# Performance work log

Measured on AMD Instinct MI355X. Metric: run time of the kernel, lower is better.

The kernel has to match this reference:

```python
import jax, jax.numpy as jnp
import numpy as np

N_HEAD = 16
D_K = 64
D_V = 64
EMBED = 1024
BATCH = 4
SEQ = 2048

def setup_inputs() -> dict:
    key = jax.random.key(0)
    ks = jax.random.split(key, 12)
    s = lambda d: 1.0 / np.sqrt(d)
    u = lambda k, shape, d: jax.random.uniform(k, shape, jnp.float32, -s(d), s(d))
    return {
        'z': jax.random.normal(ks[0], (BATCH, SEQ, EMBED), jnp.float32),
        'wq': u(ks[1], (EMBED, D_K), D_K),
        'wk': u(ks[2], (EMBED, D_K), D_K),
        'wv': u(ks[3], (EMBED, D_V), D_V),
        'fcq_w': u(ks[4], (D_K, N_HEAD * D_K), D_K),
        'fcq_b': u(ks[5], (N_HEAD * D_K,), N_HEAD * D_K),
        'fck_w': u(ks[6], (D_K, N_HEAD * D_K), D_K),
        'fck_b': u(ks[7], (N_HEAD * D_K,), N_HEAD * D_K),
        'fcv_w': u(ks[8], (D_V, N_HEAD * D_V), D_V),
        'fcv_b': u(ks[9], (N_HEAD * D_V,), N_HEAD * D_V),
        'fco_w': u(ks[10], (N_HEAD * D_V, EMBED), EMBED),
        'fco_b': u(ks[11], (EMBED,), EMBED),
    }

def reference(z, wq, wk, wv, fcq_w, fcq_b, fck_w, fck_b, fcv_w, fcv_b, fco_w, fco_b):
    b, n, _ = z.shape
    scale = jnp.sqrt(jnp.float32(D_K))
    # bottleneck projections then per-head expansion
    q = (z @ wq) @ fcq_w + fcq_b  # [b, n, H*dk]
    k = (z @ wk) @ fck_w + fck_b  # [b, n, H*dk]
    v = (z @ wv) @ fcv_w + fcv_b  # [b, n, H*dv]
    q = q.reshape(b, n, N_HEAD, D_K)
    k = k.reshape(b, n, N_HEAD, D_K)
    v = v.reshape(b, n, N_HEAD, D_V)
    scores = jnp.einsum('bihd,bjhd->bhij', q, k) / scale  # [b, H, n, n]
    attn = jax.nn.softmax(scores, axis=-1)
    out = jnp.einsum('bhij,bjhd->bihd', attn, v)  # [b, n, H, dv]
    out = out.reshape(b, n, N_HEAD * D_V)
    return out @ fco_w + fco_b  # [b, n, embed]
```

## Files before the change

kernel.cpp:

```cpp
#include <hip/hip_runtime.h>


typedef __bf16 bf16x8 __attribute__((ext_vector_type(8)));
typedef __bf16 bf16x4 __attribute__((ext_vector_type(4)));
typedef __bf16 bf16x2 __attribute__((ext_vector_type(2)));
typedef float floatx4 __attribute__((ext_vector_type(4)));
typedef float floatx16 __attribute__((ext_vector_type(16)));
typedef unsigned int uintx4 __attribute__((ext_vector_type(4)));
typedef unsigned int uintx2 __attribute__((ext_vector_type(2)));

#define SW64(row, col) (((row) << 6) | (((((col) >> 3) ^ ((row) & 7) ^ (((row) >> 3) & 7)) << 3) | ((col) & 7)))

#if __has_builtin(__builtin_amdgcn_exp2f)
__device__ __forceinline__ float fast_exp2(float x) { return __builtin_amdgcn_exp2f(x); }
#else
__device__ __forceinline__ float fast_exp2(float x) { return exp2f(x); }
#endif

__device__ __forceinline__ unsigned int pack_bf16(float lo, float hi) {
    bf16x2 w; w[0] = (__bf16)lo; w[1] = (__bf16)hi;
    return __builtin_bit_cast(unsigned int, w);
}
__device__ __forceinline__ unsigned int pack2(__bf16 lo, __bf16 hi) {
    bf16x2 w; w[0] = lo; w[1] = hi;
    return __builtin_bit_cast(unsigned int, w);
}
#if __has_builtin(__builtin_amdgcn_permlane32_swap)
__device__ __forceinline__ void xchg(unsigned int& X, unsigned int& Y, int) {
    uintx2 r = __builtin_amdgcn_permlane32_swap(X, Y, false, false);
    X = r[0]; Y = r[1];
}
#else
__device__ __forceinline__ void xchg(unsigned int& X, unsigned int& Y, int hl) {
    unsigned int sX = (unsigned int)__shfl_xor((int)X, 32);
    unsigned int sY = (unsigned int)__shfl_xor((int)Y, 32);
    unsigned int lo = hl ? sY : X;
    unsigned int hi = hl ? Y : sX;
    X = lo; Y = hi;
}
#endif
__device__ __forceinline__ bf16x8 frag4(unsigned int a, unsigned int b, unsigned int c, unsigned int d) {
    uintx4 u; u[0] = a; u[1] = b; u[2] = c; u[3] = d;
    return __builtin_bit_cast(bf16x8, u);
}
__device__ __forceinline__ void async_b128(const __bf16* g, __bf16* l) {
    __builtin_amdgcn_global_load_lds(
        (const __attribute__((address_space(1))) unsigned int*)g,
        (__attribute__((address_space(3))) unsigned int*)l, 16, 0, 0);
}

__device__ __forceinline__ bf16x8 cvt8(const void* src, int f, long idx) {
    bf16x8 v;
    if (f) {
        const float* s = (const float*)src + idx;
        float4 f0 = *(const float4*)s;
        float4 f1 = *(const float4*)(s + 4);
        v[0] = (__bf16)f0.x; v[1] = (__bf16)f0.y; v[2] = (__bf16)f0.z; v[3] = (__bf16)f0.w;
        v[4] = (__bf16)f1.x; v[5] = (__bf16)f1.y; v[6] = (__bf16)f1.z; v[7] = (__bf16)f1.w;
    } else {
        v = *(const bf16x8*)((const __bf16*)src + idx);
    }
    return v;
}

__global__ void detect_dtype(const unsigned short* __restrict__ z, int* __restrict__ flag) {
    __shared__ int cnt;
    if (threadIdx.x == 0) cnt = 0;
    __syncthreads();
    int local = 0;
    for (int i = threadIdx.x; i < 16384; i += 256) {
        unsigned int u = (unsigned int)z[i] << 16;
        float x = __uint_as_float(u);
        float ax = fabsf(x);
        if (!(ax <= 1024.0f) || (x != 0.0f && ax < 1e-20f)) local++;
    }
    atomicAdd(&cnt, local);
    __syncthreads();
    if (threadIdx.x == 0) *flag = (cnt > 1310) ? 1 : 0;
}

struct MegaArgs { const void* z; const void* bias[4]; const void* w[7]; };

__global__ __launch_bounds__(256) void mega_convert(MegaArgs a, __bf16* __restrict__ cv,
                                                    const int* __restrict__ flag) {
    const int f = *flag;
    const unsigned int blk = blockIdx.x;
    const int tid = threadIdx.x;

    if (blk < 4096) {
        const long i = ((long)blk * 256 + tid) * 8;
        *(bf16x8*)&cv[i] = cvt8(a.z, f, i);
        return;
    }
    if (blk < 4098) {
        const int idx = (((int)blk - 4096) * 256 + tid) * 8;
        const int b = idx >> 10, o = idx & 1023;
        *(bf16x8*)&cv[9830400 + b * 1024 + o] = cvt8(a.bias[b], f, o);
        return;
    }
    const int t = blk - 4098;
    int bx, by, R, C;
    const void* src;
    __bf16* dst;
    if (t < 48) {
        const int m = t >> 4; by = t & 15; bx = 0; R = 1024; C = 64;
        src = a.w[m]; dst = cv + 8388608 + m * 65536;
    } else if (t < 96) {
        const int m = (t - 48) >> 4; bx = (t - 48) & 15; by = 0; R = 64; C = 1024;
        src = a.w[3 + m]; dst = cv + 8585216 + m * 65536;
    } else {
        const int u = t - 96; bx = u & 15; by = u >> 4; R = 1024; C = 1024;
        src = a.w[6]; dst = cv + 8781824;
    }
    __shared__ __bf16 tl[64][72];
    const int r0 = by * 64, c0 = bx * 64;
    const int rr = tid >> 3, c8 = (tid & 7) << 3;
    #pragma unroll
    for (int p = 0; p < 2; p++) {
        bf16x8 v = cvt8(src, f, (long)(r0 + p * 32 + rr) * C + c0 + c8);
        #pragma unroll
        for (int j = 0; j < 8; j++) tl[c8 + j][p * 32 + rr] = v[j];
    }
    __syncthreads();
    #pragma unroll
    for (int p = 0; p < 2; p++) {
        bf16x8 v;
        #pragma unroll
        for (int j = 0; j < 8; j++) v[j] = tl[p * 32 + rr][c8 + j];
        *(bf16x8*)&dst[(long)(c0 + p * 32 + rr) * R + r0 + c8] = v;
    }
}

__global__ __launch_bounds__(256, 2) void gemm64(
    const __bf16* __restrict__ A,
    const __bf16* __restrict__ BT0, const __bf16* __restrict__ BT1, const __bf16* __restrict__ BT2,
    __bf16* __restrict__ C0, __bf16* __restrict__ C1, __bf16* __restrict__ C2,
    int K)
{
    const int zsel = blockIdx.z;
    const __bf16* BT = (zsel == 0) ? BT0 : (zsel == 1) ? BT1 : BT2;
    __bf16* C = (zsel == 0) ? C0 : (zsel == 1) ? C1 : C2;
    const int m0 = blockIdx.x * 64;
    const int tid = threadIdx.x;
    const int wave = tid >> 6, ln = tid & 63;
    const int l15 = tid & 15, quad = (tid >> 4) & 3;

    __shared__ __bf16 As[64 * 64];
    __shared__ __bf16 Bs[64 * 64];

    const int r_off = ln >> 3, j_off = ln & 7;
    floatx4 acc[4] = {};

    for (int k0 = 0; k0 < K; k0 += 64) {
        __syncthreads();
        #pragma unroll
        for (int it = 0; it < 2; it++) {
            const int seg = wave * 2 + it;
            const int row = seg * 8 + r_off;
            const int c = j_off ^ (row & 7) ^ ((row >> 3) & 7);
            async_b128(&A[(long)(m0 + row) * K + k0 + c * 8], &As[seg * 512]);
            async_b128(&BT[(long)row * K + k0 + c * 8], &Bs[seg * 512]);
        }
        __syncthreads();
        #pragma unroll
        for (int ks = 0; ks < 2; ks++) {
            bf16x8 av = *(const bf16x8*)&As[SW64(wave * 16 + l15, ks * 32 + quad * 8)];
            #pragma unroll
            for (int nt = 0; nt < 4; nt++) {
                bf16x8 bv = *(const bf16x8*)&Bs[SW64(nt * 16 + l15, ks * 32 + quad * 8)];
                acc[nt] = __builtin_amdgcn_mfma_f32_16x16x32_bf16(av, bv, acc[nt], 0, 0, 0);
            }
        }
    }
    #pragma unroll
    for (int nt = 0; nt < 4; nt++) {
        const int col = nt * 16 + l15;
        #pragma unroll
        for (int r = 0; r < 4; r++)
            C[(long)(m0 + wave * 16 + quad * 4 + r) * 64 + col] = (__bf16)acc[nt][r];
    }
}

__global__ __launch_bounds__(256, 2) void gemm128(
    const __bf16* __restrict__ A0, const __bf16* __restrict__ A1, const __bf16* __restrict__ A2,
    const __bf16* __restrict__ BT0, const __bf16* __restrict__ BT1, const __bf16* __restrict__ BT2,
    const __bf16* __restrict__ bias0, const __bf16* __restrict__ bias1, const __bf16* __restrict__ bias2,
    void* __restrict__ C0, void* __restrict__ C1, void* __restrict__ C2,
    int M, int N, int K, const int* flagp,
    float os0, float os1, float os2)
{
    const int zsel = blockIdx.z;
    const __bf16* A = (zsel == 0) ? A0 : (zsel == 1) ? A1 : A2;
    const __bf16* BT = (zsel == 0) ? BT0 : (zsel == 1) ? BT1 : BT2;
    const __bf16* bias = (zsel == 0) ? bias0 : (zsel == 1) ? bias1 : bias2;
    void* C = (zsel == 0) ? C0 : (zsel == 1) ? C1 : C2;
    const float oscale = (zsel == 0) ? os0 : (zsel == 1) ? os1 : os2;
    const int out_fp32 = flagp ? *flagp : 0;

    const int m0 = blockIdx.x * 128;
    const int n0 = blockIdx.y * 128;
    const int tid = threadIdx.x;
    const int wave = tid >> 6, ln = tid & 63;
    const int wr = wave >> 1, wc = wave & 1;
    const int l15 = tid & 15, quad = (tid >> 4) & 3;

    __shared__ __bf16 As[128 * 64];
    __shared__ __bf16 Bs[128 * 64];

    const int r_off = ln >> 3, j_off = ln & 7;

    floatx4 acc[4][4] = {};

    for (int k0 = 0; k0 < K; k0 += 64) {
        __syncthreads();
        #pragma unroll
        for (int it = 0; it < 4; it++) {
            const int seg = wave * 4 + it;
            const int row = seg * 8 + r_off;
            const int c = j_off ^ (row & 7) ^ ((row >> 3) & 7);
            async_b128(&A[(long)(m0 + row) * K + k0 + c * 8], &As[seg * 512]);
            async_b128(&BT[(long)(n0 + row) * K + k0 + c * 8], &Bs[seg * 512]);
        }
        __syncthreads();
        #pragma unroll
        for (int ks = 0; ks < 2; ks++) {
            bf16x8 a[4], b[4];
            #pragma unroll
            for (int rt = 0; rt < 4; rt++)
                a[rt] = *(const bf16x8*)&As[SW64(wr * 64 + rt * 16 + l15, ks * 32 + quad * 8)];
            #pragma unroll
            for (int nt = 0; nt < 4; nt++)
                b[nt] = *(const bf16x8*)&Bs[SW64(wc * 64 + nt * 16 + l15, ks * 32 + quad * 8)];
            #pragma unroll
            for (int rt = 0; rt < 4; rt++)
                #pragma unroll
                for (int nt = 0; nt < 4; nt++)
                    acc[rt][nt] = __builtin_amdgcn_mfma_f32_16x16x32_bf16(a[rt], b[nt], acc[rt][nt], 0, 0, 0);
        }
    }
    #pragma unroll
    for (int rt = 0; rt < 4; rt++) {
        const int row = m0 + wr * 64 + rt * 16 + quad * 4;
        #pragma unroll
        for (int nt = 0; nt < 4; nt++) {
            const int col = n0 + wc * 64 + nt * 16 + l15;
            float bv = (float)bias[col];
            #pragma unroll
            for (int r = 0; r < 4; r++) {
                float val = (acc[rt][nt][r] + bv) * oscale;
                if (out_fp32) ((float*)C)[(long)(row + r) * N + col] = val;
                else ((__bf16*)C)[(long)(row + r) * N + col] = (__bf16)val;
            }
        }
    }
}

__global__ __launch_bounds__(256, 3) void attn_kernel(
    const __bf16* __restrict__ Qg, const __bf16* __restrict__ Kg,
    const __bf16* __restrict__ Vg, __bf16* __restrict__ Og)
{
    const int bh = blockIdx.x;
    const int b = bh >> 4, h = bh & 15;
    const int q0 = blockIdx.y * 128;
    const int base = b * 2048 * 1024 + h * 64;
    const int tid = threadIdx.x;
    const int wave = tid >> 6, ln = tid & 63;
    const int l31 = ln & 31, hl = ln >> 5;
    const int h8 = hl * 8;

    __shared__ __bf16 Ks[2][64 * 64];
    __shared__ __bf16 VTs[2][64 * 64];

    bf16x8 qf[4];
    #pragma unroll
    for (int ks = 0; ks < 4; ks++)
        qf[ks] = *(const bf16x8*)&Qg[base + (q0 + wave * 32 + l31) * 1024 + ks * 16 + h8];

    const int kr = tid >> 3, kc = (tid & 7) << 3;
    const int vr2 = (tid >> 3) * 2, vc = (tid & 7) << 3;

    {
        bf16x8 ka = *(const bf16x8*)&Kg[base + kr * 1024 + kc];
        bf16x8 kb = *(const bf16x8*)&Kg[base + (kr + 32) * 1024 + kc];
        bf16x8 va = *(const bf16x8*)&Vg[base + vr2 * 1024 + vc];
        bf16x8 vb = *(const bf16x8*)&Vg[base + (vr2 + 1) * 1024 + vc];
        *(bf16x8*)&Ks[0][SW64(kr, kc)] = ka;
        *(bf16x8*)&Ks[0][SW64(kr + 32, kc)] = kb;
        #pragma unroll
        for (int j = 0; j < 8; j++)
            *(unsigned int*)&VTs[0][SW64(vc + j, vr2)] = pack2(va[j], vb[j]);
    }

    floatx16 o_acc[2] = {};
    float m_i = -1e30f, l_i = 0.0f;

    for (int t = 0; t < 32; t++) {
        const int cur = t & 1, nxt = cur ^ 1;
        bf16x8 nka, nkb, nva, nvb;
        if (t < 31) {
            const int kvn = (t + 1) * 64;
            nka = *(const bf16x8*)&Kg[base + (kvn + kr) * 1024 + kc];
            nkb = *(const bf16x8*)&Kg[base + (kvn + kr + 32) * 1024 + kc];
            nva = *(const bf16x8*)&Vg[base + (kvn + vr2) * 1024 + vc];
            nvb = *(const bf16x8*)&Vg[base + (kvn + vr2 + 1) * 1024 + vc];
        }
        __syncthreads();

        floatx16 sv[2] = {};
        #pragma unroll
        for (int ks = 0; ks < 4; ks++) {
            bf16x8 a0 = *(const bf16x8*)&Ks[cur][SW64(l31, ks * 16 + h8)];
            bf16x8 a1 = *(const bf16x8*)&Ks[cur][SW64(32 + l31, ks * 16 + h8)];
            sv[0] = __builtin_amdgcn_mfma_f32_32x32x16_bf16(a0, qf[ks], sv[0], 0, 0, 0);
            sv[1] = __builtin_amdgcn_mfma_f32_32x32x16_bf16(a1, qf[ks], sv[1], 0, 0, 0);
        }

        float m8[8];
        #pragma unroll
        for (int r = 0; r < 8; r++)
            m8[r] = fmaxf(fmaxf(sv[0][r], sv[0][r + 8]), fmaxf(sv[1][r], sv[1][r + 8]));
        float mx = fmaxf(fmaxf(fmaxf(m8[0], m8[4]), fmaxf(m8[1], m8[5])),
                         fmaxf(fmaxf(m8[2], m8[6]), fmaxf(m8[3], m8[7])));
        mx = fmaxf(mx, __shfl_xor(mx, 32));

        if (__any(mx > m_i + 8.0f)) {
            float m_new = fmaxf(m_i, mx);
            float alpha = fast_exp2(m_i - m_new);
            m_i = m_new;
            l_i *= alpha;
            #pragma unroll
            for (int dt = 0; dt < 2; dt++)
                #pragma unroll
                for (int r = 0; r < 16; r++) o_acc[dt][r] *= alpha;
        }

        float p0[16], p1[16];
        #pragma unroll
        for (int r = 0; r < 16; r++) p0[r] = fast_exp2(sv[0][r] - m_i);
        #pragma unroll
        for (int r = 0; r < 16; r++) p1[r] = fast_exp2(sv[1][r] - m_i);
        float rsA = 0.f, rsB = 0.f, rsC = 0.f, rsD = 0.f;
        #pragma unroll
        for (int r = 0; r < 16; r += 4) {
            rsA += p0[r]; rsB += p0[r + 1]; rsC += p0[r + 2]; rsD += p0[r + 3];
            rsA += p1[r]; rsB += p1[r + 1]; rsC += p1[r + 2]; rsD += p1[r + 3];
        }
        float rs = (rsA + rsB) + (rsC + rsD);
        rs += __shfl_xor(rs, 32);
        l_i += rs;

        bf16x8 pf0, pf1, pf2, pf3;
        {
            unsigned int A0 = pack_bf16(p0[0], p0[1]),  B0 = pack_bf16(p0[2], p0[3]);
            unsigned int C0 = pack_bf16(p0[4], p0[5]),  D0 = pack_bf16(p0[6], p0[7]);
            unsigned int A1 = pack_bf16(p0[8], p0[9]),  B1 = pack_bf16(p0[10], p0[11]);
            unsigned int C1 = pack_bf16(p0[12], p0[13]), D1 = pack_bf16(p0[14], p0[15]);
            xchg(A0, C0, hl); xchg(B0, D0, hl); xchg(A1, C1, hl); xchg(B1, D1, hl);
            pf0 = frag4(A0, B0, C0, D0);
            pf1 = frag4(A1, B1, C1, D1);
        }
        {
            unsigned int A0 = pack_bf16(p1[0], p1[1]),  B0 = pack_bf16(p1[2], p1[3]);
            unsigned int C0 = pack_bf16(p1[4], p1[5]),  D0 = pack_bf16(p1[6], p1[7]);
            unsigned int A1 = pack_bf16(p1[8], p1[9]),  B1 = pack_bf16(p1[10], p1[11]);
            unsigned int C1 = pack_bf16(p1[12], p1[13]), D1 = pack_bf16(p1[14], p1[15]);
            xchg(A0, C0, hl); xchg(B0, D0, hl); xchg(A1, C1, hl); xchg(B1, D1, hl);
            pf2 = frag4(A0, B0, C0, D0);
            pf3 = frag4(A1, B1, C1, D1);
        }

        if (t < 31) {
            *(bf16x8*)&Ks[nxt][SW64(kr, kc)] = nka;
            *(bf16x8*)&Ks[nxt][SW64(kr + 32, kc)] = nkb;
        }

        #pragma unroll
        for (int js = 0; js < 4; js++) {
            bf16x8 av0 = *(const bf16x8*)&VTs[cur][SW64(l31, js * 16 + h8)];
            bf16x8 av1 = *(const bf16x8*)&VTs[cur][SW64(32 + l31, js * 16 + h8)];
            bf16x8 pb = (js == 0) ? pf0 : (js == 1) ? pf1 : (js == 2) ? pf2 : pf3;
            o_acc[0] = __builtin_amdgcn_mfma_f32_32x32x16_bf16(av0, pb, o_acc[0], 0, 0, 0);
            o_acc[1] = __builtin_amdgcn_mfma_f32_32x32x16_bf16(av1, pb, o_acc[1], 0, 0, 0);
        }

        if (t < 31) {
            #pragma unroll
            for (int j = 0; j < 8; j++)
                *(unsigned int*)&VTs[nxt][SW64(vc + j, vr2)] = pack2(nva[j], nvb[j]);
        }
    }

    float inv = 1.0f / l_i;
    const int orow = q0 + wave * 32 + l31;
    #pragma unroll
    for (int dt = 0; dt < 2; dt++)
        #pragma unroll
        for (int g = 0; g < 4; g++) {
            bf16x4 ov;
            #pragma unroll
            for (int e = 0; e < 4; e++) ov[e] = (__bf16)(o_acc[dt][g * 4 + e] * inv);
            *(bf16x4*)&Og[base + orow * 1024 + dt * 32 + g * 8 + hl * 4] = ov;
        }
}

extern "C" void kernel_launch(void* const* d_in, const int* in_sizes, int n_in,
                              void* d_out, int out_size, void* d_ws, size_t ws_size,
                              hipStream_t stream)
{
    int* flag = (int*)d_ws;
    __bf16* cv = (__bf16*)((char*)d_ws + 256);

    const int Z = 0, WQT = 8388608, FCWT = 8585216, FCOWT = 8781824, BIAS = 9830400;
    __bf16* zb = cv + 10485760;
    __bf16* Qw = cv + 12582912;
    __bf16* Kw = Qw + 8388608;
    __bf16* Vw = Kw + 8388608;
    __bf16* Ow = cv + Z;

    detect_dtype<<<1, 256, 0, stream>>>((const unsigned short*)d_in[0], flag);

    MegaArgs ma;
    ma.z = d_in[0];
    ma.bias[0] = d_in[5]; ma.bias[1] = d_in[7]; ma.bias[2] = d_in[9]; ma.bias[3] = d_in[11];
    ma.w[0] = d_in[1]; ma.w[1] = d_in[2]; ma.w[2] = d_in[3];
    ma.w[3] = d_in[4]; ma.w[4] = d_in[6]; ma.w[5] = d_in[8];
    ma.w[6] = d_in[10];
    mega_convert<<<dim3(4450, 1), 256, 0, stream>>>(ma, cv, flag);

    gemm64<<<dim3(128, 1, 3), 256, 0, stream>>>(
        cv + Z, cv + WQT, cv + WQT + 65536, cv + WQT + 131072,
        zb, zb + 524288, zb + 1048576, 1024);

    const float QSC = 0.125f * 1.44269504088896f;
    gemm128<<<dim3(64, 8, 3), 256, 0, stream>>>(
        zb, zb + 524288, zb + 1048576,
        cv + FCWT, cv + FCWT + 65536, cv + FCWT + 131072,
        cv + BIAS, cv + BIAS + 1024, cv + BIAS + 2048,
        Qw, Kw, Vw, 8192, 1024, 64, nullptr,
        QSC, 1.0f, 1.0f);

    attn_kernel<<<dim3(64, 16), 256, 0, stream>>>(Qw, Kw, Vw, Ow);

    gemm128<<<dim3(64, 8, 1), 256, 0, stream>>>(
        Ow, Ow, Ow, cv + FCOWT, cv + FCOWT, cv + FCOWT,
        cv + BIAS + 3072, cv + BIAS + 3072, cv + BIAS + 3072,
        d_out, d_out, d_out, 8192, 1024, 1024, flag,
        1.0f, 1.0f, 1.0f);
}
```

Baseline: 267.5 us.

## Fuse three bottleneck projections into one GEMM, coarsen z conversion, interleave softmax packing

```diff
diff --git a/kernel.cpp b/kernel.cpp
--- a/kernel.cpp
+++ b/kernel.cpp
@@ -87,18 +87,22 @@
     const unsigned int blk = blockIdx.x;
     const int tid = threadIdx.x;
 
-    if (blk < 4096) {
-        const long i = ((long)blk * 256 + tid) * 8;
-        *(bf16x8*)&cv[i] = cvt8(a.z, f, i);
+    if (blk < 1024) {
+        const long base = (long)blk * 8192 + tid * 8;
+        #pragma unroll
+        for (int p = 0; p < 4; p++) {
+            const long i = base + p * 2048;
+            *(bf16x8*)&cv[i] = cvt8(a.z, f, i);
+        }
         return;
     }
-    if (blk < 4098) {
-        const int idx = (((int)blk - 4096) * 256 + tid) * 8;
+    if (blk < 1026) {
+        const int idx = (((int)blk - 1024) * 256 + tid) * 8;
         const int b = idx >> 10, o = idx & 1023;
         *(bf16x8*)&cv[9830400 + b * 1024 + o] = cvt8(a.bias[b], f, o);
         return;
     }
-    const int t = blk - 4098;
+    const int t = blk - 1026;
     int bx, by, R, C;
     const void* src;
     __bf16* dst;
@@ -131,53 +135,60 @@
     }
 }
 
-__global__ __launch_bounds__(256, 2) void gemm64(
-    const __bf16* __restrict__ A,
-    const __bf16* __restrict__ BT0, const __bf16* __restrict__ BT1, const __bf16* __restrict__ BT2,
+__global__ __launch_bounds__(256, 2) void gemm64x3(
+    const __bf16* __restrict__ A, const __bf16* __restrict__ BT,
     __bf16* __restrict__ C0, __bf16* __restrict__ C1, __bf16* __restrict__ C2,
     int K)
 {
-    const int zsel = blockIdx.z;
-    const __bf16* BT = (zsel == 0) ? BT0 : (zsel == 1) ? BT1 : BT2;
-    __bf16* C = (zsel == 0) ? C0 : (zsel == 1) ? C1 : C2;
     const int m0 = blockIdx.x * 64;
     const int tid = threadIdx.x;
     const int wave = tid >> 6, ln = tid & 63;
     const int l15 = tid & 15, quad = (tid >> 4) & 3;
 
     __shared__ __bf16 As[64 * 64];
-    __shared__ __bf16 Bs[64 * 64];
+    __shared__ __bf16 Bs[3][64 * 64];
 
     const int r_off = ln >> 3, j_off = ln & 7;
-    floatx4 acc[4] = {};
+    floatx4 acc[3][4] = {};
 
     for (int k0 = 0; k0 < K; k0 += 64) {
         __syncthreads();
         #pragma unroll
-        for (int it = 0; it < 2; it++) {
-            const int seg = wave * 2 + it;
+        for (int it = 0; it < 8; it++) {
+            const int s = wave * 8 + it;
+            const int seg = s & 7;
             const int row = seg * 8 + r_off;
             const int c = j_off ^ (row & 7) ^ ((row >> 3) & 7);
-            async_b128(&A[(long)(m0 + row) * K + k0 + c * 8], &As[seg * 512]);
-            async_b128(&BT[(long)row * K + k0 + c * 8], &Bs[seg * 512]);
+            if (s < 8)
+                async_b128(&A[(long)(m0 + row) * K + k0 + c * 8], &As[seg * 512]);
+            else {
+                const int z = (s - 8) >> 3;
+                async_b128(&BT[(long)z * 65536 + (long)row * K + k0 + c * 8], &Bs[z][seg * 512]);
+            }
         }
         __syncthreads();
         #pragma unroll
         for (int ks = 0; ks < 2; ks++) {
             bf16x8 av = *(const bf16x8*)&As[SW64(wave * 16 + l15, ks * 32 + quad * 8)];
             #pragma unroll
-            for (int nt = 0; nt < 4; nt++) {
-                bf16x8 bv = *(const bf16x8*)&Bs[SW64(nt * 16 + l15, ks * 32 + quad * 8)];
-                acc[nt] = __builtin_amdgcn_mfma_f32_16x16x32_bf16(av, bv, acc[nt], 0, 0, 0);
-            }
-        }
-    }
-    #pragma unroll
-    for (int nt = 0; nt < 4; nt++) {
-        const int col = nt * 16 + l15;
-        #pragma unroll
-        for (int r = 0; r < 4; r++)
-            C[(long)(m0 + wave * 16 + quad * 4 + r) * 64 + col] = (__bf16)acc[nt][r];
+            for (int z = 0; z < 3; z++)
+                #pragma unroll
+                for (int nt = 0; nt < 4; nt++) {
+                    bf16x8 bv = *(const bf16x8*)&Bs[z][SW64(nt * 16 + l15, ks * 32 + quad * 8)];
+                    acc[z][nt] = __builtin_amdgcn_mfma_f32_16x16x32_bf16(av, bv, acc[z][nt], 0, 0, 0);
+                }
+        }
+    }
+    #pragma unroll
+    for (int z = 0; z < 3; z++) {
+        __bf16* C = (z == 0) ? C0 : (z == 1) ? C1 : C2;
+        #pragma unroll
+        for (int nt = 0; nt < 4; nt++) {
+            const int col = nt * 16 + l15;
+            #pragma unroll
+            for (int r = 0; r < 4; r++)
+                C[(long)(m0 + wave * 16 + quad * 4 + r) * 64 + col] = (__bf16)acc[z][nt][r];
+        }
     }
 }
 
@@ -318,9 +329,11 @@
         float m8[8];
         #pragma unroll
         for (int r = 0; r < 8; r++)
-            m8[r] = fmaxf(fmaxf(sv[0][r], sv[0][r + 8]), fmaxf(sv[1][r], sv[1][r + 8]));
-        float mx = fmaxf(fmaxf(fmaxf(m8[0], m8[4]), fmaxf(m8[1], m8[5])),
-                         fmaxf(fmaxf(m8[2], m8[6]), fmaxf(m8[3], m8[7])));
+            m8[r] = fmaxf(fmaxf(fmaxf(sv[0][r], sv[0][r + 8]), sv[1][r]), sv[1][r + 8]);
+        float ma = fmaxf(fmaxf(m8[0], m8[1]), m8[2]);
+        float mb = fmaxf(fmaxf(m8[3], m8[4]), m8[5]);
+        float mc = fmaxf(fmaxf(m8[6], m8[7]), ma);
+        float mx = fmaxf(mb, mc);
         mx = fmaxf(mx, __shfl_xor(mx, 32));
 
         if (__any(mx > m_i + 8.0f)) {
@@ -334,40 +347,26 @@
                 for (int r = 0; r < 16; r++) o_acc[dt][r] *= alpha;
         }
 
-        float p0[16], p1[16];
-        #pragma unroll
-        for (int r = 0; r < 16; r++) p0[r] = fast_exp2(sv[0][r] - m_i);
-        #pragma unroll
-        for (int r = 0; r < 16; r++) p1[r] = fast_exp2(sv[1][r] - m_i);
         float rsA = 0.f, rsB = 0.f, rsC = 0.f, rsD = 0.f;
-        #pragma unroll
-        for (int r = 0; r < 16; r += 4) {
-            rsA += p0[r]; rsB += p0[r + 1]; rsC += p0[r + 2]; rsD += p0[r + 3];
-            rsA += p1[r]; rsB += p1[r + 1]; rsC += p1[r + 2]; rsD += p1[r + 3];
-        }
+        bf16x8 pf0, pf1, pf2, pf3;
+        #define PGROUP(SVV, BASE, PF) { \
+            float e0 = fast_exp2(SVV[BASE + 0] - m_i), e1 = fast_exp2(SVV[BASE + 1] - m_i); \
+            float e2 = fast_exp2(SVV[BASE + 2] - m_i), e3 = fast_exp2(SVV[BASE + 3] - m_i); \
+            float e4 = fast_exp2(SVV[BASE + 4] - m_i), e5 = fast_exp2(SVV[BASE + 5] - m_i); \
+            float e6 = fast_exp2(SVV[BASE + 6] - m_i), e7 = fast_exp2(SVV[BASE + 7] - m_i); \
+            rsA += e0 + e4; rsB += e1 + e5; rsC += e2 + e6; rsD += e3 + e7; \
+            unsigned int Aw = pack_bf16(e0, e1), Bw = pack_bf16(e2, e3); \
+            unsigned int Cw = pack_bf16(e4, e5), Dw = pack_bf16(e6, e7); \
+            xchg(Aw, Cw, hl); xchg(Bw, Dw, hl); \
+            PF = frag4(Aw, Bw, Cw, Dw); }
+        PGROUP(sv[0], 0, pf0)
+        PGROUP(sv[0], 8, pf1)
+        PGROUP(sv[1], 0, pf2)
+        PGROUP(sv[1], 8, pf3)
+        #undef PGROUP
         float rs = (rsA + rsB) + (rsC + rsD);
         rs += __shfl_xor(rs, 32);
         l_i += rs;
-
-        bf16x8 pf0, pf1, pf2, pf3;
-        {
-            unsigned int A0 = pack_bf16(p0[0], p0[1]),  B0 = pack_bf16(p0[2], p0[3]);
-            unsigned int C0 = pack_bf16(p0[4], p0[5]),  D0 = pack_bf16(p0[6], p0[7]);
-            unsigned int A1 = pack_bf16(p0[8], p0[9]),  B1 = pack_bf16(p0[10], p0[11]);
-            unsigned int C1 = pack_bf16(p0[12], p0[13]), D1 = pack_bf16(p0[14], p0[15]);
-            xchg(A0, C0, hl); xchg(B0, D0, hl); xchg(A1, C1, hl); xchg(B1, D1, hl);
-            pf0 = frag4(A0, B0, C0, D0);
-            pf1 = frag4(A1, B1, C1, D1);
-        }
-        {
-            unsigned int A0 = pack_bf16(p1[0], p1[1]),  B0 = pack_bf16(p1[2], p1[3]);
-            unsigned int C0 = pack_bf16(p1[4], p1[5]),  D0 = pack_bf16(p1[6], p1[7]);
-            unsigned int A1 = pack_bf16(p1[8], p1[9]),  B1 = pack_bf16(p1[10], p1[11]);
-            unsigned int C1 = pack_bf16(p1[12], p1[13]), D1 = pack_bf16(p1[14], p1[15]);
-            xchg(A0, C0, hl); xchg(B0, D0, hl); xchg(A1, C1, hl); xchg(B1, D1, hl);
-            pf2 = frag4(A0, B0, C0, D0);
-            pf3 = frag4(A1, B1, C1, D1);
-        }
 
         if (t < 31) {
             *(bf16x8*)&Ks[nxt][SW64(kr, kc)] = nka;
@@ -425,11 +424,10 @@
     ma.w[0] = d_in[1]; ma.w[1] = d_in[2]; ma.w[2] = d_in[3];
     ma.w[3] = d_in[4]; ma.w[4] = d_in[6]; ma.w[5] = d_in[8];
     ma.w[6] = d_in[10];
-    mega_convert<<<dim3(4450, 1), 256, 0, stream>>>(ma, cv, flag);
-
-    gemm64<<<dim3(128, 1, 3), 256, 0, stream>>>(
-        cv + Z, cv + WQT, cv + WQT + 65536, cv + WQT + 131072,
-        zb, zb + 524288, zb + 1048576, 1024);
+    mega_convert<<<dim3(1378, 1), 256, 0, stream>>>(ma, cv, flag);
+
+    gemm64x3<<<dim3(128, 1, 1), 256, 0, stream>>>(
+        cv + Z, cv + WQT, zb, zb + 524288, zb + 1048576, 1024);
 
     const float QSC = 0.125f * 1.44269504088896f;
     gemm128<<<dim3(64, 8, 3), 256, 0, stream>>>(
```

Measured after the change: 275.5 us. 3.0% more time.
